# Performance work log

Measured on AMD Instinct MI355X. Metric: run time of the kernel, lower is better.

## Reference

```python
import jax, jax.numpy as jnp
import numpy as np

N = 50000
NUM_NEIGHBORS = 16
E = N * NUM_NEIGHBORS
NDIM_IN, EDIM, NDIM_OUT = 128, 64, 128


def setup_inputs() -> dict:
    key = jax.random.key(0)
    k1, k2, k3, k4, k5, k6, k7 = jax.random.split(key, 7)
    nfeats = jax.random.normal(k1, (N, 1, NDIM_IN), dtype=jnp.float32)
    efeats = jax.random.normal(k2, (E, 1, EDIM), dtype=jnp.float32)
    W_msg = jax.random.normal(k3, (NDIM_OUT, NDIM_IN + EDIM), dtype=jnp.float32) * 0.05
    b_msg = jax.random.normal(k4, (NDIM_OUT,), dtype=jnp.float32) * 0.05
    W_apply = jax.random.normal(k5, (NDIM_OUT, NDIM_IN + NDIM_OUT), dtype=jnp.float32) * 0.05
    b_apply = jax.random.normal(k6, (NDIM_OUT,), dtype=jnp.float32) * 0.05
    src_idx = jax.random.randint(k7, (E,), 0, N, dtype=jnp.int32)
    # sampled graph: each node is the destination of exactly NUM_NEIGHBORS edges
    dst_idx = jnp.repeat(jnp.arange(N, dtype=jnp.int32), NUM_NEIGHBORS)
    return {"nfeats": nfeats, "efeats": efeats, "W_msg": W_msg, "b_msg": b_msg,
            "W_apply": W_apply, "b_apply": b_apply, "src_idx": src_idx, "dst_idx": dst_idx}


def reference(nfeats, efeats, W_msg, b_msg, W_apply, b_apply, src_idx, dst_idx):
    n = nfeats.shape[0]
    # message: W_msg(cat([src_h, edge_h], -1))  -> [E, 1, ndim_out]
    src_h = nfeats[src_idx]                                   # [E,1,Din] gather
    msg_in = jnp.concatenate([src_h, efeats], axis=-1)        # [E,1,Din+Edim]
    m = jnp.einsum('eid,od->eio', msg_in, W_msg) + b_msg      # [E,1,Dout]
    # mean aggregation over incoming edges per destination node
    msum = jax.ops.segment_sum(m[:, 0, :], dst_idx, num_segments=n)   # [N,Dout]
    cnt = jax.ops.segment_sum(jnp.ones((m.shape[0],), m.dtype), dst_idx, num_segments=n)
    h_neigh = (msum / jnp.maximum(cnt, 1.0)[:, None])[:, None, :]     # [N,1,Dout]
    # apply: relu(W_apply(cat([nfeats, h_neigh], -1)))
    app_in = jnp.concatenate([nfeats, h_neigh], axis=-1)      # [N,1,Din+Dout]
    h_new = jax.nn.relu(jnp.einsum('nid,od->nio', app_in, W_apply) + b_apply)
    return h_new
```

## Files before the change

kernel.cpp:

```cpp
#include <hip/hip_runtime.h>

#define N_NODES 50000
#define NN 16
#define K_FUSED 320
#define NP 50048

typedef __attribute__((ext_vector_type(8))) short bfrag8;
typedef __attribute__((ext_vector_type(4))) float facc4;

__device__ __forceinline__ unsigned short f2bf(float f) {
    unsigned int u = __builtin_bit_cast(unsigned int, f);
    u = (u + 0x7fffu + ((u >> 16) & 1u)) >> 16;
    return (unsigned short)u;
}

__global__ void wfuse_kernel(const float* __restrict__ W_msg,
                             const float* __restrict__ b_msg,
                             const float* __restrict__ W_apply,
                             const float* __restrict__ b_apply,
                             unsigned short* __restrict__ Wf,
                             float* __restrict__ bias_f) {
    __shared__ float sWa[128];
    const int o = blockIdx.x;
    const int tid = threadIdx.x;
    if (tid < 128) sWa[tid] = W_apply[o * 256 + 128 + tid];
    __syncthreads();
    if (tid < 128) Wf[o * K_FUSED + tid] = f2bf(W_apply[o * 256 + tid]);
    if (tid < 192) {
        float acc = 0.f;
        #pragma unroll 8
        for (int p = 0; p < 128; ++p) acc += sWa[p] * W_msg[p * 192 + tid];
        Wf[o * K_FUSED + 128 + tid] = f2bf(acc);
    } else if (tid == 192) {
        float acc = b_apply[o];
        for (int p = 0; p < 128; ++p) acc += sWa[p] * b_msg[p];
        bias_f[o] = acc;
    }
}

__global__ __launch_bounds__(256)
void prep_kernel(const float* __restrict__ nfeats,
                 const float* __restrict__ efeats,
                 const int* __restrict__ src_idx,
                 unsigned short* __restrict__ X) {
    const int wave = threadIdx.x >> 6;
    const int lane = threadIdx.x & 63;
    const int n = blockIdx.x * 4 + wave;
    if (n >= N_NODES) return;
    const long e0 = (long)n * NN;

    float s0 = 0.f, s1 = 0.f;
    float tacc = 0.f;
    #pragma unroll
    for (int j = 0; j < NN; ++j) {
        const int src = src_idx[e0 + j];
        const float2 v = *(const float2*)(nfeats + (long)src * 128 + 2 * lane);
        s0 += v.x; s1 += v.y;
        tacc += efeats[(e0 + j) * 64 + lane];
    }
    const float inv = 1.f / 16.f;
    s0 *= inv; s1 *= inv; tacc *= inv;

    const float2 xv = *(const float2*)(nfeats + (long)n * 128 + 2 * lane);
    unsigned short* row = X + (long)n * K_FUSED;
    ((unsigned int*)row)[lane] =
        (unsigned)f2bf(xv.x) | ((unsigned)f2bf(xv.y) << 16);
    ((unsigned int*)(row + 128))[lane] =
        (unsigned)f2bf(s0) | ((unsigned)f2bf(s1) << 16);
    row[256 + lane] = f2bf(tacc);
}

__global__ __launch_bounds__(512)
void apply_kernel(const unsigned short* __restrict__ X,
                  const uint4* __restrict__ WfQ,
                  const float* __restrict__ bias_f,
                  float* __restrict__ out) {
    __shared__ uint4 ldsW[64 * 41];
    const int bx = blockIdx.x;
    const int mblk = bx >> 1;
    const int nhalf = bx & 1;
    const int tid = threadIdx.x;

    #pragma unroll
    for (int i = tid; i < 64 * 40; i += 512) {
        const int r = i / 40, q = i - r * 40;
        ldsW[r * 41 + q] = WfQ[(nhalf * 64 + r) * 40 + q];
    }
    __syncthreads();

    const int wave = tid >> 6, lane = tid & 63;
    const int quad = lane >> 4, mcol = lane & 15;
    const int node0 = mblk * 128 + wave * 16;
    const char* arow = (const char*)(X + (long)(node0 + mcol) * K_FUSED);
    const char* ldsB = (const char*)ldsW;

    facc4 acc[4] = {};
    #pragma unroll
    for (int ks = 0; ks < 10; ++ks) {
        const uint4 av = *(const uint4*)(arow + ks * 64 + quad * 16);
        const bfrag8 a = __builtin_bit_cast(bfrag8, av);
        #pragma unroll
        for (int t = 0; t < 4; ++t) {
            const int nrow = t * 16 + mcol;
            const uint4 bv = *(const uint4*)(ldsB + nrow * 656 + ks * 64 + quad * 16);
            const bfrag8 b = __builtin_bit_cast(bfrag8, bv);
            acc[t] = __builtin_amdgcn_mfma_f32_16x16x32_bf16(a, b, acc[t], 0, 0, 0);
        }
    }

    #pragma unroll
    for (int t = 0; t < 4; ++t) {
        const int ocol = nhalf * 64 + t * 16 + mcol;
        const float bb = bias_f[ocol];
        #pragma unroll
        for (int r = 0; r < 4; ++r) {
            const int node = node0 + quad * 4 + r;
            if (node < N_NODES) {
                const float v = acc[t][r] + bb;
                out[(long)node * 128 + ocol] = v > 0.f ? v : 0.f;
            }
        }
    }
}

extern "C" void kernel_launch(void* const* d_in, const int* in_sizes, int n_in,
                              void* d_out, int out_size, void* d_ws, size_t ws_size,
                              hipStream_t stream) {
    const float* nfeats  = (const float*)d_in[0];
    const float* efeats  = (const float*)d_in[1];
    const float* W_msg   = (const float*)d_in[2];
    const float* b_msg   = (const float*)d_in[3];
    const float* W_apply = (const float*)d_in[4];
    const float* b_apply = (const float*)d_in[5];
    const int*   src_idx = (const int*)d_in[6];
    float* out = (float*)d_out;

    char* ws = (char*)d_ws;
    unsigned short* Wf     = (unsigned short*)ws;
    float*          bias_f = (float*)(ws + 81920);
    unsigned short* X      = (unsigned short*)(ws + 82432);

    wfuse_kernel<<<128, 256, 0, stream>>>(W_msg, b_msg, W_apply, b_apply, Wf, bias_f);
    prep_kernel<<<(N_NODES + 3) / 4, 256, 0, stream>>>(nfeats, efeats, src_idx, X);
    apply_kernel<<<(NP / 128) * 2, 512, 0, stream>>>(X, (const uint4*)Wf, bias_f, out);
}
```

Measured before the change: 351.6 us.

## Pre-convert node features to bf16 and vectorize neighbor gather and edge reduction

Adds a conversion kernel that writes node features as bf16 into a compact table and into the X self-feature slot, so the neighbor gather reads half as many bytes per source row. The src indices are loaded once per wave and broadcast with readlane, replacing 16 scalar loads. Edge features are read as float4 with a cross-lane shuffle reduction. The trade-off is an extra launch, an extra pass over nfeats, and rounding neighbor features to bf16 before averaging, which slightly changes numerics.

```diff
diff --git a/kernel.cpp b/kernel.cpp
--- a/kernel.cpp
+++ b/kernel.cpp
@@ -12,6 +12,12 @@
     unsigned int u = __builtin_bit_cast(unsigned int, f);
     u = (u + 0x7fffu + ((u >> 16) & 1u)) >> 16;
     return (unsigned short)u;
+}
+__device__ __forceinline__ float bf2f(unsigned int u16) {
+    return __builtin_bit_cast(float, u16 << 16);
+}
+__device__ __forceinline__ unsigned int pack2(unsigned short lo, unsigned short hi) {
+    return (unsigned int)lo | ((unsigned int)hi << 16);
 }
 
 __global__ void wfuse_kernel(const float* __restrict__ W_msg,
@@ -39,7 +45,21 @@
 }
 
 __global__ __launch_bounds__(256)
-void prep_kernel(const float* __restrict__ nfeats,
+void cvt_kernel(const float* __restrict__ nfeats,
+                unsigned short* __restrict__ X,
+                unsigned short* __restrict__ nbf) {
+    const int idx = blockIdx.x * 256 + threadIdx.x;
+    const int n = idx >> 5, d = (idx & 31) * 4;
+    const float4 v = *(const float4*)(nfeats + (long)n * 128 + d);
+    uint2 p;
+    p.x = pack2(f2bf(v.x), f2bf(v.y));
+    p.y = pack2(f2bf(v.z), f2bf(v.w));
+    *(uint2*)(nbf + (long)n * 128 + d) = p;
+    *(uint2*)(X + (long)n * K_FUSED + d) = p;
+}
+
+__global__ __launch_bounds__(256)
+void prep_kernel(const unsigned short* __restrict__ nbf,
                  const float* __restrict__ efeats,
                  const int* __restrict__ src_idx,
                  unsigned short* __restrict__ X) {
@@ -49,25 +69,43 @@
     if (n >= N_NODES) return;
     const long e0 = (long)n * NN;
 
+    const int myidx = src_idx[e0 + (lane & 15)];
+
     float s0 = 0.f, s1 = 0.f;
-    float tacc = 0.f;
     #pragma unroll
     for (int j = 0; j < NN; ++j) {
-        const int src = src_idx[e0 + j];
-        const float2 v = *(const float2*)(nfeats + (long)src * 128 + 2 * lane);
-        s0 += v.x; s1 += v.y;
-        tacc += efeats[(e0 + j) * 64 + lane];
+        const int src = __builtin_amdgcn_readlane(myidx, j);
+        const unsigned int v =
+            *(const unsigned int*)(nbf + (long)src * 128 + 2 * lane);
+        s0 += bf2f(v & 0xffffu);
+        s1 += bf2f(v >> 16);
     }
+
+    const float4* eb = (const float4*)(efeats + e0 * 64);
+    float t0 = 0.f, t1 = 0.f, t2 = 0.f, t3 = 0.f;
+    #pragma unroll
+    for (int it = 0; it < 4; ++it) {
+        const float4 v = eb[it * 64 + lane];
+        t0 += v.x; t1 += v.y; t2 += v.z; t3 += v.w;
+    }
+    #pragma unroll
+    for (int off = 16; off <= 32; off <<= 1) {
+        t0 += __shfl_xor(t0, off);
+        t1 += __shfl_xor(t1, off);
+        t2 += __shfl_xor(t2, off);
+        t3 += __shfl_xor(t3, off);
+    }
+
     const float inv = 1.f / 16.f;
-    s0 *= inv; s1 *= inv; tacc *= inv;
-
-    const float2 xv = *(const float2*)(nfeats + (long)n * 128 + 2 * lane);
     unsigned short* row = X + (long)n * K_FUSED;
-    ((unsigned int*)row)[lane] =
-        (unsigned)f2bf(xv.x) | ((unsigned)f2bf(xv.y) << 16);
     ((unsigned int*)(row + 128))[lane] =
-        (unsigned)f2bf(s0) | ((unsigned)f2bf(s1) << 16);
-    row[256 + lane] = f2bf(tacc);
+        pack2(f2bf(s0 * inv), f2bf(s1 * inv));
+    if (lane < 16) {
+        uint2 p;
+        p.x = pack2(f2bf(t0 * inv), f2bf(t1 * inv));
+        p.y = pack2(f2bf(t2 * inv), f2bf(t3 * inv));
+        *(uint2*)(row + 256 + 4 * lane) = p;
+    }
 }
 
 __global__ __launch_bounds__(512)
@@ -139,8 +177,10 @@
     unsigned short* Wf     = (unsigned short*)ws;
     float*          bias_f = (float*)(ws + 81920);
     unsigned short* X      = (unsigned short*)(ws + 82432);
+    unsigned short* nbf    = (unsigned short*)(ws + 82432 + (size_t)NP * K_FUSED * 2);
 
     wfuse_kernel<<<128, 256, 0, stream>>>(W_msg, b_msg, W_apply, b_apply, Wf, bias_f);
-    prep_kernel<<<(N_NODES + 3) / 4, 256, 0, stream>>>(nfeats, efeats, src_idx, X);
+    cvt_kernel<<<(N_NODES * 32) / 256, 256, 0, stream>>>(nfeats, X, nbf);
+    prep_kernel<<<(N_NODES + 3) / 4, 256, 0, stream>>>(nbf, efeats, src_idx, X);
     apply_kernel<<<(NP / 128) * 2, 512, 0, stream>>>(X, (const uint4*)Wf, bias_f, out);
 }
```

Measured after the change: 352.2 us. About the same (+0.2%).
